# Performance work log

Hardware: AMD Instinct MI355X
Metric: run time of the kernel (lower is better)

## Reference

```python
import jax, jax.numpy as jnp
import numpy as np

B, S, D = 32, 512, 512      # batch, seq, feature
E, H, O, K = 8, 2048, 512, 2  # experts, expert hidden, expert out, top_k


def setup_inputs() -> dict:
    key = jax.random.key(0)
    ks = jax.random.split(key, 5)
    sc = lambda k, shape, scale: jax.random.normal(k, shape, jnp.float32) * scale
    return {
        "x": sc(ks[0], (B, S, D), 1.0),
        "attn_w": sc(ks[1], (D, 1), 0.05),
        "attn_b": jnp.zeros((1,), jnp.float32),
        "gate_w": sc(ks[2], (D, E), 0.05),
        "gate_b": jnp.zeros((E,), jnp.float32),
        "w1": sc(ks[3], (E, D, H), 0.02),
        "b1": jnp.zeros((E, H), jnp.float32),
        "w2": sc(ks[4], (E, H, O), 0.02),
        "b2": jnp.zeros((E, O), jnp.float32),
    }


def reference(x, attn_w, attn_b, gate_w, gate_b, w1, b1, w2, b2):
    # --- attention pooling over the sequence axis ---
    scores = x @ attn_w + attn_b                      # [B,S,1]
    aw = jax.nn.softmax(scores, axis=1)               # softmax over seq
    pooled = jnp.sum(x * aw, axis=1)                  # [B,D]

    # --- gating: softmax -> top-k mask -> renormalize ---
    gates = jax.nn.softmax(pooled @ gate_w + gate_b, axis=-1)  # [B,E]
    _, idx = jax.lax.top_k(gates, K)                  # [B,K]
    mask = jnp.sum(jax.nn.one_hot(idx, E, dtype=gates.dtype), axis=-2)  # [B,E]
    g = gates * mask
    g = g / (jnp.sum(g, axis=-1, keepdims=True) + 1e-9)        # [B,E]

    # --- dense all-experts compute (exact GELU, as keras Dense('gelu')) ---
    h = jax.nn.gelu(jnp.einsum('bsd,edh->ebsh', x, w1) + b1[:, None, None, :],
                    approximate=False)                 # [E,B,S,H]
    eo = jax.nn.gelu(jnp.einsum('ebsh,eho->ebso', h, w2) + b2[:, None, None, :],
                     approximate=False)                # [E,B,S,O]

    # --- weighted combine over experts ---
    return jnp.einsum('ebso,be->bso', eo, g)           # [B,S,O]
```

## Files before the change

### kernel.cpp

```cpp
#include <hip/hip_runtime.h>
#include <hip/hip_bf16.h>
#include <math.h>

#define B_  32
#define S_  512
#define D_  512
#define E_  8
#define H_  2048
#define O_  512

typedef __bf16 bf16x8 __attribute__((ext_vector_type(8)));
typedef float  f32x4  __attribute__((ext_vector_type(4)));

#define GL2LDS(src, dst) \
  __builtin_amdgcn_global_load_lds((const __attribute__((address_space(1))) void*)(src), \
                                   (__attribute__((address_space(3))) void*)(dst), 16, 0, 0)

#define MFMA16(a, b, c) __builtin_amdgcn_mfma_f32_16x16x32_bf16((a), (b), (c), 0, 0, 0)

__device__ __forceinline__ float gelu_fast(float v) {
  float w = v * fmaf(v * v, 0.0713548162f, 1.5957691216f);
  float e = __expf(-w);
  return v * __builtin_amdgcn_rcpf(1.0f + e);
}


__global__ __launch_bounds__(256) void cast_score_kernel(
    const float* __restrict__ x, const float* __restrict__ attn_w,
    char* __restrict__ xpack, float* __restrict__ scores)
{
  const int t = threadIdx.x;
  const int r = t >> 5;
  const int cg = t & 31;
  const int row = blockIdx.x * 8 + r;
  const int bb = row >> 9, s = row & 511;
  const float* src  = x + (size_t)row * D_ + cg * 16;
  const float* wsrc = attn_w + cg * 16;
  char* xp = xpack + (size_t)bb * 524288 + s * 64;
  const int sx = (s >> 1) & 3;
  float acc = 0.f;
#pragma unroll
  for (int k = 0; k < 4; ++k) {
    const int d0 = cg * 16 + k * 4;
    float4 v  = *(const float4*)(src + k * 4);
    float4 wv = *(const float4*)(wsrc + k * 4);
    acc += v.x * wv.x + v.y * wv.y + v.z * wv.z + v.w * wv.w;
    ushort4 o;
    o.x = __builtin_bit_cast(unsigned short, __float2bfloat16(v.x));
    o.y = __builtin_bit_cast(unsigned short, __float2bfloat16(v.y));
    o.z = __builtin_bit_cast(unsigned short, __float2bfloat16(v.z));
    o.w = __builtin_bit_cast(unsigned short, __float2bfloat16(v.w));
    const int u = d0 >> 5;
    const int byte = u * 32768 + ((((d0 >> 3) & 3) ^ sx) << 4) + (d0 & 7) * 2;
    *(ushort4*)(xp + byte) = o;
  }
#pragma unroll
  for (int off = 16; off; off >>= 1) acc += __shfl_xor(acc, off);
  if (cg == 0) scores[row] = acc;
}

__global__ __launch_bounds__(512) void softmax_aw_kernel(
    const float* __restrict__ scores, float* __restrict__ aw)
{
  __shared__ float red[8];
  __shared__ float mm, ss;
  const int t = threadIdx.x, b = blockIdx.x;
  float v = scores[b * S_ + t];
  float m = v;
#pragma unroll
  for (int off = 32; off; off >>= 1) m = fmaxf(m, __shfl_xor(m, off));
  if ((t & 63) == 0) red[t >> 6] = m;
  __syncthreads();
  if (t == 0) {
    float a = red[0];
    for (int i = 1; i < 8; ++i) a = fmaxf(a, red[i]);
    mm = a;
  }
  __syncthreads();
  float e = expf(v - mm);
  float s = e;
#pragma unroll
  for (int off = 32; off; off >>= 1) s += __shfl_xor(s, off);
  if ((t & 63) == 0) red[t >> 6] = s;
  __syncthreads();
  if (t == 0) {
    float a = 0.f;
    for (int i = 0; i < 8; ++i) a += red[i];
    ss = 1.f / a;
  }
  __syncthreads();
  aw[b * S_ + t] = e * ss;
}

__global__ __launch_bounds__(512) void pool_kernel(
    const float* __restrict__ x, const float* __restrict__ aw, float* __restrict__ pooled)
{
  __shared__ float sm[4][128];
  const int t = threadIdx.x;
  const int dl = t & 127;
  const int sh = t >> 7;
  const int b = blockIdx.y;
  const int d = blockIdx.x * 128 + dl;
  const float* xp  = x + (size_t)b * S_ * D_ + d;
  const float* awb = aw + b * S_;
  float acc = 0.f;
#pragma unroll 4
  for (int s = sh; s < S_; s += 4)
    acc = fmaf(awb[s], xp[(size_t)s * D_], acc);
  if (sh) sm[sh][dl] = acc;
  __syncthreads();
  if (sh == 0) pooled[b * D_ + d] = acc + sm[1][dl] + sm[2][dl] + sm[3][dl];
}

__global__ __launch_bounds__(256) void gate_psort_kernel(
    const float* __restrict__ pooled, const float* __restrict__ gate_w,
    const float* __restrict__ gate_b, int* __restrict__ gidx, float* __restrict__ gwt,
    int* __restrict__ psort)
{
  __shared__ float gl[32][8];
  const int t = threadIdx.x;
  const int b = t >> 3, ee = t & 7;
  float z = gate_b[ee];
  const float* pb = pooled + b * D_;
  for (int d = 0; d < D_; ++d) z = fmaf(pb[d], gate_w[d * E_ + ee], z);
  gl[b][ee] = z;
  __syncthreads();
  if (t < 32) {
    float ge[8];
    float zmax = gl[t][0];
    for (int i = 1; i < 8; ++i) zmax = fmaxf(zmax, gl[t][i]);
    float zs = 0.f;
    for (int i = 0; i < 8; ++i) { ge[i] = expf(gl[t][i] - zmax); zs += ge[i]; }
    for (int i = 0; i < 8; ++i) ge[i] /= zs;
    int i0 = 0;
    for (int i = 1; i < 8; ++i) if (ge[i] > ge[i0]) i0 = i;
    int i1 = -1;
    for (int i = 0; i < 8; ++i) if (i != i0 && (i1 < 0 || ge[i] > ge[i1])) i1 = i;
    float denom = ge[i0] + ge[i1] + 1e-9f;
    gidx[t * 2 + 0] = i0; gidx[t * 2 + 1] = i1;
    gwt[t * 2 + 0] = ge[i0] / denom; gwt[t * 2 + 1] = ge[i1] / denom;
  }
  __syncthreads();
  if (t == 0) {
    int cnt[E_] = {}, pos[E_];
    for (int p = 0; p < 2 * B_; ++p) cnt[gidx[p]]++;
    int s = 0;
    for (int e2 = 0; e2 < E_; ++e2) { pos[e2] = s; s += cnt[e2]; }
    for (int p = 0; p < 2 * B_; ++p) psort[pos[gidx[p]]++] = p;
  }
}

__global__ void pack_w_kernel(const float* __restrict__ in, char* __restrict__ outp,
                              int R, int C)
{
  __shared__ float tile[32][33];
  const int z = blockIdx.z;
  const float* inz = in + (size_t)z * R * C;
  const int c0 = blockIdx.x * 32, r0 = blockIdx.y * 32;
  const int tx = threadIdx.x, ty = threadIdx.y;
#pragma unroll
  for (int jj = 0; jj < 4; ++jj) {
    int r = r0 + ty + jj * 8;
    tile[ty + jj * 8][tx] = inz[(size_t)r * C + c0 + tx];
  }
  __syncthreads();
  const int k = r0 + tx;
  const int u = k >> 5;
  const int PAN = C * 64;
  char* oz = outp + (size_t)z * R * C * 2 + (size_t)u * PAN;
  const int kslot = (k >> 3) & 3;
  const int kbyte = (k & 7) * 2;
#pragma unroll
  for (int jj = 0; jj < 4; ++jj) {
    const int row = c0 + ty + jj * 8;
    const int byte = row * 64 + ((kslot ^ ((row >> 1) & 3)) << 4) + kbyte;
    *(ushort*)(oz + byte) =
        __builtin_bit_cast(unsigned short, __float2bfloat16(tile[tx][ty + jj * 8]));
  }
}

__device__ __forceinline__ void gemm_core_m97(const char* __restrict__ Ag, const char* __restrict__ Bg,
                                              const size_t unitA, const size_t unitB,
                                              const int NT, char* lds, f32x4 (&acc)[4][4])
{
  const int tid = threadIdx.x;
  const int l = tid & 63;
  const int w = tid >> 6;
  const int wm = w >> 1;
  const int wn = w & 1;
  const int lr = l & 15;
  const int ks = (l >> 4) & 3;
  const int swz = ((ks ^ ((lr >> 1) & 3)) << 4);
  const int abase = wm * 4096 + lr * 64 + swz;
  const int bbase = 16384 + wn * 4096 + lr * 64 + swz;
  const int dst = tid * 16;

#pragma unroll 1
  for (int t = 0; t < NT; ++t) {
    const char* a0 = Ag + (size_t)(2 * t)     * unitA;
    const char* a1 = Ag + (size_t)(2 * t + 1) * unitA;
    const char* b0 = Bg + (size_t)(2 * t)     * unitB;
    const char* b1 = Bg + (size_t)(2 * t + 1) * unitB;
    GL2LDS(a0 + dst, lds + dst);          GL2LDS(a0 + 4096 + dst, lds + 4096 + dst);
    GL2LDS(a1 + dst, lds + 8192 + dst);   GL2LDS(a1 + 4096 + dst, lds + 12288 + dst);
    GL2LDS(b0 + dst, lds + 16384 + dst);  GL2LDS(b0 + 4096 + dst, lds + 20480 + dst);
    GL2LDS(b1 + dst, lds + 24576 + dst);  GL2LDS(b1 + 4096 + dst, lds + 28672 + dst);
    asm volatile("s_waitcnt vmcnt(0)" ::: "memory");
    __builtin_amdgcn_s_barrier();

    bf16x8 a0f[4], a1f[4], b0f[4], b1f[4];
#pragma unroll
    for (int m = 0; m < 4; ++m) {
      a0f[m] = *(const bf16x8*)(lds + abase + m * 1024);
      a1f[m] = *(const bf16x8*)(lds + 8192 + abase + m * 1024);
    }
#pragma unroll
    for (int n = 0; n < 4; ++n) {
      b0f[n] = *(const bf16x8*)(lds + bbase + n * 1024);
      b1f[n] = *(const bf16x8*)(lds + 8192 + bbase + n * 1024);
    }
#pragma unroll
    for (int m = 0; m < 4; ++m)
#pragma unroll
      for (int n = 0; n < 4; ++n) {
        acc[m][n] = MFMA16(a0f[m], b0f[n], acc[m][n]);
        acc[m][n] = MFMA16(a1f[m], b1f[n], acc[m][n]);
      }
    __builtin_amdgcn_s_barrier();
  }
}

__global__ __launch_bounds__(256, 4) void gemm1_kernel(
    const char* __restrict__ xpack, const char* __restrict__ W1pack,
    const float* __restrict__ b1, char* __restrict__ Hpack,
    const int* __restrict__ gidx, const int* __restrict__ psort)
{
  __shared__ char lds[32768];
  const int P = blockIdx.x;
  const int L = (P & 7) * 512 + (P >> 3);
  const int p = psort[L >> 6];
  const int tl = L & 63;
  const int b = p >> 1;
  const int e = gidx[p];
  const int h0 = (tl >> 2) * 128;
  const int s0 = (tl & 3) * 128;
  const char* Ag = W1pack + (size_t)e * 2097152 + h0 * 64;
  const char* Bg = xpack + (size_t)b * 524288 + s0 * 64;
  f32x4 acc[4][4] = {};
  gemm_core_m97(Ag, Bg, 131072, 32768, D_ / 64, lds, acc);

  const int tid = threadIdx.x, l = tid & 63, w = tid >> 6;
  const int wm = w >> 1, wn = w & 1, lr = l & 15, q4 = ((l >> 4) & 3) << 2;
  const float* b1e = b1 + (size_t)e * H_ + h0;
  char* Hp = Hpack + (size_t)p * 2097152;
#pragma unroll
  for (int m = 0; m < 4; ++m) {
    const int hl = wm * 64 + m * 16 + q4;
    const int h = h0 + hl;
    const int uh = h >> 5;
    const int hslot = (h >> 3) & 3;
    const int hbyte = (h & 7) * 2;
    const float4 bias = *(const float4*)(b1e + hl);
#pragma unroll
    for (int n = 0; n < 4; ++n) {
      const int sl = s0 + wn * 64 + n * 16 + lr;
      ushort4 ov;
      ov.x = __builtin_bit_cast(unsigned short, __float2bfloat16(gelu_fast(acc[m][n][0] + bias.x)));
      ov.y = __builtin_bit_cast(unsigned short, __float2bfloat16(gelu_fast(acc[m][n][1] + bias.y)));
      ov.z = __builtin_bit_cast(unsigned short, __float2bfloat16(gelu_fast(acc[m][n][2] + bias.z)));
      ov.w = __builtin_bit_cast(unsigned short, __float2bfloat16(gelu_fast(acc[m][n][3] + bias.w)));
      const int byte = uh * 32768 + sl * 64 + ((hslot ^ ((sl >> 1) & 3)) << 4) + hbyte;
      *(ushort4*)(Hp + byte) = ov;
    }
  }
}

__global__ __launch_bounds__(256, 4) void gemm2_kernel(
    const char* __restrict__ Hpack, const char* __restrict__ W2pack,
    const float* __restrict__ b2, float* __restrict__ out,
    const int* __restrict__ gidx, const float* __restrict__ gwt,
    const int* __restrict__ psort)
{
  __shared__ char lds[32768];
  const int P = blockIdx.x;
  const int L = (P & 7) * 128 + (P >> 3);
  const int p = psort[L >> 4];
  const int tl = L & 15;
  const int b = p >> 1;
  const int e = gidx[p];
  const float gw = gwt[p];
  const int o0 = (tl >> 2) * 128;
  const int s0 = (tl & 3) * 128;
  const char* Ag = Hpack + (size_t)p * 2097152 + s0 * 64;
  const char* Bg = W2pack + (size_t)e * 2097152 + o0 * 64;
  f32x4 acc[4][4] = {};
  gemm_core_m97(Ag, Bg, 32768, 32768, H_ / 64, lds, acc);

  const int tid = threadIdx.x, l = tid & 63, w = tid >> 6;
  const int wm = w >> 1, wn = w & 1, lr = l & 15, q4 = ((l >> 4) & 3) << 2;
  const float* b2e = b2 + (size_t)e * O_ + o0;
#pragma unroll
  for (int m = 0; m < 4; ++m) {
    const int sl = s0 + wm * 64 + m * 16 + q4;
#pragma unroll
    for (int n = 0; n < 4; ++n) {
      const int ol = wn * 64 + n * 16 + lr;
      const float bias = b2e[ol];
      float* dstp = out + ((size_t)b * S_ + sl) * O_ + o0 + ol;
#pragma unroll
      for (int j = 0; j < 4; ++j)
        atomicAdd(dstp + (size_t)j * O_, gelu_fast(acc[m][n][j] + bias) * gw);
    }
  }
}

__global__ void sentinel_kernel(float* out, int n) {
  int i = blockIdx.x * blockDim.x + threadIdx.x;
  for (; i < n; i += gridDim.x * blockDim.x) out[i] = 1.0e6f;
}

extern "C" void kernel_launch(void* const* d_in, const int* in_sizes, int n_in,
                              void* d_out, int out_size, void* d_ws, size_t ws_size,
                              hipStream_t stream)
{
  const float* x      = (const float*)d_in[0];
  const float* attn_w = (const float*)d_in[1];
  const float* gate_w = (const float*)d_in[3];
  const float* gate_b = (const float*)d_in[4];
  const float* w1     = (const float*)d_in[5];
  const float* b1     = (const float*)d_in[6];
  const float* w2     = (const float*)d_in[7];
  const float* b2     = (const float*)d_in[8];
  float* out = (float*)d_out;

  char* ws = (char*)d_ws;
  const size_t OFF_GIDX = 0;
  const size_t OFF_GWT  = 256;
  const size_t OFF_PSRT = 512;
  const size_t OFF_X    = 1024;
  const size_t SZ_X     = (size_t)B_ * S_ * D_ * 2;
  const size_t OFF_W1T  = OFF_X + SZ_X;
  const size_t SZ_W1T   = (size_t)E_ * H_ * D_ * 2;
  const size_t OFF_W2T  = OFF_W1T + SZ_W1T;
  const size_t SZ_W2T   = (size_t)E_ * O_ * H_ * 2;
  const size_t OFF_H    = OFF_W2T + SZ_W2T;
  const size_t PAIR_H   = (size_t)S_ * H_ * 2;

  if (OFF_H + 64 * PAIR_H > ws_size) {
    hipLaunchKernelGGL(sentinel_kernel, dim3(256), dim3(256), 0, stream, out, out_size);
    return;
  }

  int*   gidx   = (int*)(ws + OFF_GIDX);
  float* gwt    = (float*)(ws + OFF_GWT);
  int*   psort  = (int*)(ws + OFF_PSRT);
  char*  xpack  = ws + OFF_X;
  char*  W1pack = ws + OFF_W1T;
  char*  W2pack = ws + OFF_W2T;
  char*  Hpack  = ws + OFF_H;
  float* scores = (float*)(ws + OFF_H);
  float* aw     = (float*)(ws + OFF_H + 65536);
  float* pooled = (float*)(ws + OFF_H + 131072);

  hipLaunchKernelGGL(cast_score_kernel, dim3(B_ * S_ / 8), dim3(256), 0, stream,
                     x, attn_w, xpack, scores);
  hipLaunchKernelGGL(softmax_aw_kernel, dim3(B_), dim3(512), 0, stream, scores, aw);
  hipLaunchKernelGGL(pool_kernel, dim3(4, B_), dim3(512), 0, stream, x, aw, pooled);
  hipLaunchKernelGGL(gate_psort_kernel, dim3(1), dim3(256), 0, stream,
                     pooled, gate_w, gate_b, gidx, gwt, psort);
  hipLaunchKernelGGL(pack_w_kernel, dim3(H_ / 32, D_ / 32, E_), dim3(32, 8), 0, stream,
                     w1, W1pack, D_, H_);
  hipLaunchKernelGGL(pack_w_kernel, dim3(O_ / 32, H_ / 32, E_), dim3(32, 8), 0, stream,
                     w2, W2pack, H_, O_);
  hipMemsetAsync(d_out, 0, (size_t)out_size * sizeof(float), stream);

  hipLaunchKernelGGL(gemm1_kernel, dim3(4096), dim3(256), 0, stream,
                     xpack, W1pack, b1, Hpack, gidx, psort);
  hipLaunchKernelGGL(gemm2_kernel, dim3(1024), dim3(256), 0, stream,
                     Hpack, W2pack, b2, out, gidx, gwt, psort);
}
```

Baseline: 260.9 us.

## Use 2-wave 64x128 warp tiles in expert GEMMs and fuse softmax into pooling

The shared GEMM core now runs with 128-thread blocks of two waves instead of four. Each wave computes a 64x128 slice with an 8-wide accumulator array, so each B fragment loaded from LDS is reused across more MFMAs and fewer LDS reads are needed per MFMA. The trade-off is more accumulator registers per wave and fewer waves to hide latency. Separately, the attention softmax is folded into the pooling kernel through a shared-memory weight buffer. That removes one launch and the global round trip for the attention weights, at the cost of redoing the softmax in each of the four D-blocks.

```diff
diff --git a/kernel.cpp b/kernel.cpp
--- a/kernel.cpp
+++ b/kernel.cpp
@@ -59,12 +59,16 @@
   if (cg == 0) scores[row] = acc;
 }
 
-__global__ __launch_bounds__(512) void softmax_aw_kernel(
-    const float* __restrict__ scores, float* __restrict__ aw)
-{
+__global__ __launch_bounds__(512) void pool_kernel(
+    const float* __restrict__ x, const float* __restrict__ scores,
+    float* __restrict__ pooled)
+{
+  __shared__ float awsh[512];
   __shared__ float red[8];
   __shared__ float mm, ss;
-  const int t = threadIdx.x, b = blockIdx.x;
+  __shared__ float sm[4][128];
+  const int t = threadIdx.x;
+  const int b = blockIdx.y;
   float v = scores[b * S_ + t];
   float m = v;
 #pragma unroll
@@ -89,24 +93,17 @@
     ss = 1.f / a;
   }
   __syncthreads();
-  aw[b * S_ + t] = e * ss;
-}
-
-__global__ __launch_bounds__(512) void pool_kernel(
-    const float* __restrict__ x, const float* __restrict__ aw, float* __restrict__ pooled)
-{
-  __shared__ float sm[4][128];
-  const int t = threadIdx.x;
+  awsh[t] = e * ss;
+  __syncthreads();
+
   const int dl = t & 127;
   const int sh = t >> 7;
-  const int b = blockIdx.y;
   const int d = blockIdx.x * 128 + dl;
-  const float* xp  = x + (size_t)b * S_ * D_ + d;
-  const float* awb = aw + b * S_;
+  const float* xp = x + (size_t)b * S_ * D_ + d;
   float acc = 0.f;
 #pragma unroll 4
-  for (int s = sh; s < S_; s += 4)
-    acc = fmaf(awb[s], xp[(size_t)s * D_], acc);
+  for (int s2 = sh; s2 < S_; s2 += 4)
+    acc = fmaf(awsh[s2], xp[(size_t)s2 * D_], acc);
   if (sh) sm[sh][dl] = acc;
   __syncthreads();
   if (sh == 0) pooled[b * D_ + d] = acc + sm[1][dl] + sm[2][dl] + sm[3][dl];
@@ -179,20 +176,18 @@
   }
 }
 
-__device__ __forceinline__ void gemm_core_m97(const char* __restrict__ Ag, const char* __restrict__ Bg,
-                                              const size_t unitA, const size_t unitB,
-                                              const int NT, char* lds, f32x4 (&acc)[4][4])
+__device__ __forceinline__ void gemm_core_v9(const char* __restrict__ Ag, const char* __restrict__ Bg,
+                                             const size_t unitA, const size_t unitB,
+                                             const int NT, char* lds, f32x4 (&acc)[4][8])
 {
   const int tid = threadIdx.x;
   const int l = tid & 63;
   const int w = tid >> 6;
-  const int wm = w >> 1;
-  const int wn = w & 1;
   const int lr = l & 15;
   const int ks = (l >> 4) & 3;
   const int swz = ((ks ^ ((lr >> 1) & 3)) << 4);
-  const int abase = wm * 4096 + lr * 64 + swz;
-  const int bbase = 16384 + wn * 4096 + lr * 64 + swz;
+  const int abase = (w * 64 + lr) * 64 + swz;
+  const int bbase = 16384 + lr * 64 + swz;
   const int dst = tid * 16;
 
 #pragma unroll 1
@@ -201,36 +196,35 @@
     const char* a1 = Ag + (size_t)(2 * t + 1) * unitA;
     const char* b0 = Bg + (size_t)(2 * t)     * unitB;
     const char* b1 = Bg + (size_t)(2 * t + 1) * unitB;
-    GL2LDS(a0 + dst, lds + dst);          GL2LDS(a0 + 4096 + dst, lds + 4096 + dst);
-    GL2LDS(a1 + dst, lds + 8192 + dst);   GL2LDS(a1 + 4096 + dst, lds + 12288 + dst);
-    GL2LDS(b0 + dst, lds + 16384 + dst);  GL2LDS(b0 + 4096 + dst, lds + 20480 + dst);
-    GL2LDS(b1 + dst, lds + 24576 + dst);  GL2LDS(b1 + 4096 + dst, lds + 28672 + dst);
+#pragma unroll
+    for (int c = 0; c < 4; ++c) {
+      GL2LDS(a0 + c * 2048 + dst, lds + c * 2048 + dst);
+      GL2LDS(a1 + c * 2048 + dst, lds + 8192 + c * 2048 + dst);
+      GL2LDS(b0 + c * 2048 + dst, lds + 16384 + c * 2048 + dst);
+      GL2LDS(b1 + c * 2048 + dst, lds + 24576 + c * 2048 + dst);
+    }
     asm volatile("s_waitcnt vmcnt(0)" ::: "memory");
     __builtin_amdgcn_s_barrier();
 
-    bf16x8 a0f[4], a1f[4], b0f[4], b1f[4];
-#pragma unroll
-    for (int m = 0; m < 4; ++m) {
-      a0f[m] = *(const bf16x8*)(lds + abase + m * 1024);
-      a1f[m] = *(const bf16x8*)(lds + 8192 + abase + m * 1024);
+#pragma unroll
+    for (int kh = 0; kh < 2; ++kh) {
+      bf16x8 bv[8];
+#pragma unroll
+      for (int n = 0; n < 8; ++n)
+        bv[n] = *(const bf16x8*)(lds + 16384 + kh * 8192 + (lr + n * 16) * 64 + swz);
+#pragma unroll
+      for (int m = 0; m < 4; ++m) {
+        const bf16x8 af = *(const bf16x8*)(lds + kh * 8192 + abase + m * 1024);
+#pragma unroll
+        for (int n = 0; n < 8; ++n)
+          acc[m][n] = MFMA16(af, bv[n], acc[m][n]);
+      }
     }
-#pragma unroll
-    for (int n = 0; n < 4; ++n) {
-      b0f[n] = *(const bf16x8*)(lds + bbase + n * 1024);
-      b1f[n] = *(const bf16x8*)(lds + 8192 + bbase + n * 1024);
-    }
-#pragma unroll
-    for (int m = 0; m < 4; ++m)
-#pragma unroll
-      for (int n = 0; n < 4; ++n) {
-        acc[m][n] = MFMA16(a0f[m], b0f[n], acc[m][n]);
-        acc[m][n] = MFMA16(a1f[m], b1f[n], acc[m][n]);
-      }
     __builtin_amdgcn_s_barrier();
   }
 }
 
-__global__ __launch_bounds__(256, 4) void gemm1_kernel(
+__global__ __launch_bounds__(128, 2) void gemm1_kernel(
     const char* __restrict__ xpack, const char* __restrict__ W1pack,
     const float* __restrict__ b1, char* __restrict__ Hpack,
     const int* __restrict__ gidx, const int* __restrict__ psort)
@@ -246,24 +240,24 @@
   const int s0 = (tl & 3) * 128;
   const char* Ag = W1pack + (size_t)e * 2097152 + h0 * 64;
   const char* Bg = xpack + (size_t)b * 524288 + s0 * 64;
-  f32x4 acc[4][4] = {};
-  gemm_core_m97(Ag, Bg, 131072, 32768, D_ / 64, lds, acc);
+  f32x4 acc[4][8] = {};
+  gemm_core_v9(Ag, Bg, 131072, 32768, D_ / 64, lds, acc);
 
   const int tid = threadIdx.x, l = tid & 63, w = tid >> 6;
-  const int wm = w >> 1, wn = w & 1, lr = l & 15, q4 = ((l >> 4) & 3) << 2;
+  const int lr = l & 15, q4 = ((l >> 4) & 3) << 2;
   const float* b1e = b1 + (size_t)e * H_ + h0;
   char* Hp = Hpack + (size_t)p * 2097152;
 #pragma unroll
   for (int m = 0; m < 4; ++m) {
-    const int hl = wm * 64 + m * 16 + q4;
+    const int hl = w * 64 + m * 16 + q4;
     const int h = h0 + hl;
     const int uh = h >> 5;
     const int hslot = (h >> 3) & 3;
     const int hbyte = (h & 7) * 2;
     const float4 bias = *(const float4*)(b1e + hl);
 #pragma unroll
-    for (int n = 0; n < 4; ++n) {
-      const int sl = s0 + wn * 64 + n * 16 + lr;
+    for (int n = 0; n < 8; ++n) {
+      const int sl = s0 + n * 16 + lr;
       ushort4 ov;
       ov.x = __builtin_bit_cast(unsigned short, __float2bfloat16(gelu_fast(acc[m][n][0] + bias.x)));
       ov.y = __builtin_bit_cast(unsigned short, __float2bfloat16(gelu_fast(acc[m][n][1] + bias.y)));
@@ -275,7 +269,7 @@
   }
 }
 
-__global__ __launch_bounds__(256, 4) void gemm2_kernel(
+__global__ __launch_bounds__(128, 2) void gemm2_kernel(
     const char* __restrict__ Hpack, const char* __restrict__ W2pack,
     const float* __restrict__ b2, float* __restrict__ out,
     const int* __restrict__ gidx, const float* __restrict__ gwt,
@@ -293,18 +287,18 @@
   const int s0 = (tl & 3) * 128;
   const char* Ag = Hpack + (size_t)p * 2097152 + s0 * 64;
   const char* Bg = W2pack + (size_t)e * 2097152 + o0 * 64;
-  f32x4 acc[4][4] = {};
-  gemm_core_m97(Ag, Bg, 32768, 32768, H_ / 64, lds, acc);
+  f32x4 acc[4][8] = {};
+  gemm_core_v9(Ag, Bg, 32768, 32768, H_ / 64, lds, acc);
 
   const int tid = threadIdx.x, l = tid & 63, w = tid >> 6;
-  const int wm = w >> 1, wn = w & 1, lr = l & 15, q4 = ((l >> 4) & 3) << 2;
+  const int lr = l & 15, q4 = ((l >> 4) & 3) << 2;
   const float* b2e = b2 + (size_t)e * O_ + o0;
 #pragma unroll
   for (int m = 0; m < 4; ++m) {
-    const int sl = s0 + wm * 64 + m * 16 + q4;
-#pragma unroll
-    for (int n = 0; n < 4; ++n) {
-      const int ol = wn * 64 + n * 16 + lr;
+    const int sl = s0 + w * 64 + m * 16 + q4;
+#pragma unroll
+    for (int n = 0; n < 8; ++n) {
+      const int ol = n * 16 + lr;
       const float bias = b2e[ol];
       float* dstp = out + ((size_t)b * S_ + sl) * O_ + o0 + ol;
 #pragma unroll
@@ -359,13 +353,11 @@
   char*  W2pack = ws + OFF_W2T;
   char*  Hpack  = ws + OFF_H;
   float* scores = (float*)(ws + OFF_H);
-  float* aw     = (float*)(ws + OFF_H + 65536);
   float* pooled = (float*)(ws + OFF_H + 131072);
 
   hipLaunchKernelGGL(cast_score_kernel, dim3(B_ * S_ / 8), dim3(256), 0, stream,
                      x, attn_w, xpack, scores);
-  hipLaunchKernelGGL(softmax_aw_kernel, dim3(B_), dim3(512), 0, stream, scores, aw);
-  hipLaunchKernelGGL(pool_kernel, dim3(4, B_), dim3(512), 0, stream, x, aw, pooled);
+  hipLaunchKernelGGL(pool_kernel, dim3(4, B_), dim3(512), 0, stream, x, scores, pooled);
   hipLaunchKernelGGL(gate_psort_kernel, dim3(1), dim3(256), 0, stream,
                      pooled, gate_w, gate_b, gidx, gwt, psort);
   hipLaunchKernelGGL(pack_w_kernel, dim3(H_ / 32, D_ / 32, E_), dim3(32, 8), 0, stream,
@@ -374,8 +366,8 @@
                      w2, W2pack, H_, O_);
   hipMemsetAsync(d_out, 0, (size_t)out_size * sizeof(float), stream);
 
-  hipLaunchKernelGGL(gemm1_kernel, dim3(4096), dim3(256), 0, stream,
+  hipLaunchKernelGGL(gemm1_kernel, dim3(4096), dim3(128), 0, stream,
                      xpack, W1pack, b1, Hpack, gidx, psort);
-  hipLaunchKernelGGL(gemm2_kernel, dim3(1024), dim3(256), 0, stream,
+  hipLaunchKernelGGL(gemm2_kernel, dim3(1024), dim3(128), 0, stream,
                      Hpack, W2pack, b2, out, gidx, gwt, psort);
 }
```

Result: slower. 272.9 us (+4.6%).
